# Kernel optimization log

Measured on AMD Instinct MI355X. Metric: run time of the kernel, lower is better.

## Reference

```python
import jax, jax.numpy as jnp
import numpy as np

IN, H, FC1, FC2, OUT = 3, 30, 64, 32, 1
B, T = 8192, 256


def _lstm_layer(xT, W_ih, W_hh, b_ih, b_hh):
    """xT: (T, B, Din). Returns (hidden sequence (T,B,H), final h (B,H)).
    PyTorch gate order: i, f, g, o."""
    # Precompute input contribution for all timesteps (one big GEMM).
    gx = jnp.einsum('tbd,gd->tbg', xT, W_ih) + b_ih + b_hh  # (T,B,4H)
    b = xT.shape[1]
    h0 = jnp.zeros((b, W_hh.shape[1]), xT.dtype)
    c0 = h0

    def step(carry, g):
        h, c = carry
        gates = g + h @ W_hh.T
        i, f, gg, o = jnp.split(gates, 4, axis=-1)
        i = jax.nn.sigmoid(i)
        f = jax.nn.sigmoid(f)
        gg = jnp.tanh(gg)
        o = jax.nn.sigmoid(o)
        c = f * c + i * gg
        h = o * jnp.tanh(c)
        return (h, c), h

    (h_n, _), ys = jax.lax.scan(step, (h0, c0), gx)
    return ys, h_n


def setup_inputs() -> dict:
    key = jax.random.key(0)
    ks = jax.random.split(key, 16)
    s = 0.18  # ~1/sqrt(hidden_size), matches PyTorch uniform init scale
    inp = {
        'x': jax.random.normal(ks[0], (B, T, IN), jnp.float32),
        'W_ih0': jax.random.normal(ks[1], (4 * H, IN), jnp.float32) * s,
        'W_hh0': jax.random.normal(ks[2], (4 * H, H), jnp.float32) * s,
        'b_ih0': jax.random.normal(ks[3], (4 * H,), jnp.float32) * s,
        'b_hh0': jax.random.normal(ks[4], (4 * H,), jnp.float32) * s,
        'W_ih1': jax.random.normal(ks[5], (4 * H, H), jnp.float32) * s,
        'W_hh1': jax.random.normal(ks[6], (4 * H, H), jnp.float32) * s,
        'b_ih1': jax.random.normal(ks[7], (4 * H,), jnp.float32) * s,
        'b_hh1': jax.random.normal(ks[8], (4 * H,), jnp.float32) * s,
        'W_fc1': jax.random.normal(ks[9], (FC1, H), jnp.float32) * s,
        'b_fc1': jax.random.normal(ks[10], (FC1,), jnp.float32) * s,
        'W_fc2': jax.random.normal(ks[11], (FC2, FC1), jnp.float32) * 0.125,
        'b_fc2': jax.random.normal(ks[12], (FC2,), jnp.float32) * 0.125,
        'W_fc3': jax.random.normal(ks[13], (OUT, FC2), jnp.float32) * 0.17,
        'b_fc3': jax.random.normal(ks[14], (OUT,), jnp.float32) * 0.17,
    }
    return inp


def reference(x, W_ih0, W_hh0, b_ih0, b_hh0, W_ih1, W_hh1, b_ih1, b_hh1,
              W_fc1, b_fc1, W_fc2, b_fc2, W_fc3, b_fc3):
    xT = jnp.swapaxes(x, 0, 1)  # (T,B,IN)
    ys, _ = _lstm_layer(xT, W_ih0, W_hh0, b_ih0, b_hh0)   # layer 0 sequence
    _, h_n = _lstm_layer(ys, W_ih1, W_hh1, b_ih1, b_hh1)  # layer 1 final h
    # FC head (dropout = identity in eval mode)
    z = jax.nn.relu(h_n @ W_fc1.T + b_fc1)
    z = jax.nn.relu(z @ W_fc2.T + b_fc2)
    z = jax.nn.sigmoid(z @ W_fc3.T + b_fc3)
    return z.squeeze(-1)  # (B,)
```

## Files before the change

### kernel.cpp

```cpp
#include <hip/hip_runtime.h>

#define TT   256
#define HID  30
#define LOG2E 1.4426950408889634f
#define HS   56

typedef __bf16 bf16x8_t __attribute__((ext_vector_type(8)));
typedef float  f32x4_t  __attribute__((ext_vector_type(4)));

__device__ __forceinline__ float fexp2(float x){
#if __has_builtin(__builtin_amdgcn_exp2f)
    return __builtin_amdgcn_exp2f(x);
#else
    return exp2f(x);
#endif
}
__device__ __forceinline__ float frcp(float x){
#if __has_builtin(__builtin_amdgcn_rcpf)
    return __builtin_amdgcn_rcpf(x);
#else
    return 1.f/x;
#endif
}
__device__ __forceinline__ float fsigmoid(float x){ return frcp(1.f + fexp2(-LOG2E*x)); }
__device__ __forceinline__ float ftanh_f(float x){ return 2.f*frcp(1.f + fexp2(-2.f*LOG2E*x)) - 1.f; }
__device__ __forceinline__ f32x4_t exp4(f32x4_t v){
    f32x4_t e; e[0]=fexp2(v[0]); e[1]=fexp2(v[1]); e[2]=fexp2(v[2]); e[3]=fexp2(v[3]); return e;
}
__device__ __forceinline__ f32x4_t rcp4(f32x4_t v){
    f32x4_t r; r[0]=frcp(v[0]); r[1]=frcp(v[1]); r[2]=frcp(v[2]); r[3]=frcp(v[3]); return r;
}

__global__ __launch_bounds__(512, 4)
void lstm_fused(const float* __restrict__ x,
    const float* __restrict__ Wih0, const float* __restrict__ Whh0,
    const float* __restrict__ bih0, const float* __restrict__ bhh0,
    const float* __restrict__ Wih1, const float* __restrict__ Whh1,
    const float* __restrict__ bih1, const float* __restrict__ bhh1,
    const float* __restrict__ Wfc1, const float* __restrict__ bfc1,
    const float* __restrict__ Wfc2, const float* __restrict__ bfc2,
    const float* __restrict__ Wfc3, const float* __restrict__ bfc3,
    float* __restrict__ out)
{
    __shared__ __align__(16) __bf16 h0f[2][16][HS];
    __shared__ __align__(16) __bf16 h1f[2][16][HS];
    __shared__ float h1_last[16*32];
    __shared__ float zbuf[16*64];
    __shared__ float z2buf[16*32];

    const int tid  = threadIdx.x;
    const int lane = tid & 63;
    const int wvf  = tid >> 6;
    const bool grpA = (wvf < 4);
    const int wv   = wvf & 3;
    const int n    = lane & 15;
    const int q    = lane >> 4;
    const int nl   = n & 7;
    const int u    = wv*8 + nl;
    const int hi   = n >> 3;
    const bool colok = (u < HID);
    const int bbase = blockIdx.x * 16;

    const int uq  = colok ? u : 0;
    const int wr0 = (hi ? 1 : 0)*HID + uq;
    const int wr1 = (hi ? 3 : 2)*HID + uq;

    bf16x8_t fbA{}, fbB{}, fbC{}, fbD{};
    float b0=0.f, b1=0.f, wx20=0.f, wx21=0.f;
    if (grpA) {
        #pragma unroll
        for (int j = 0; j < 8; ++j) {
            int k = q*8 + j;
            float v0=0.f, v1=0.f;
            if (colok) {
                if (k < HID) { v0 = Whh0[wr0*HID+k];      v1 = Whh0[wr1*HID+k]; }
                else         { v0 = Wih0[wr0*3+(k-HID)];  v1 = Wih0[wr1*3+(k-HID)]; }
            }
            fbA[j]=(__bf16)v0; fbB[j]=(__bf16)v1;
        }
        if (colok) {
            b0 = bih0[wr0] + bhh0[wr0];
            b1 = bih0[wr1] + bhh0[wr1];
            wx20 = Wih0[wr0*3+2];  wx21 = Wih0[wr1*3+2];
        }
    } else {
        #pragma unroll
        for (int j = 0; j < 8; ++j) {
            int k = q*8 + j;
            float v0=0.f, v1=0.f, v2=0.f, v3=0.f;
            if (colok && k < HID) {
                v0 = Wih1[wr0*HID+k];  v1 = Wih1[wr1*HID+k];
                v2 = Whh1[wr0*HID+k];  v3 = Whh1[wr1*HID+k];
            }
            fbA[j]=(__bf16)v0; fbB[j]=(__bf16)v1;
            fbC[j]=(__bf16)v2; fbD[j]=(__bf16)v3;
        }
        if (colok) {
            b0 = bih1[wr0] + bhh1[wr0];
            b1 = bih1[wr1] + bhh1[wr1];
        }
    }
    const f32x4_t bv0 = {b0,b0,b0,b0};
    const f32x4_t bv1 = {b1,b1,b1,b1};
    const float mco1 = (hi==0) ? (-2.f*LOG2E) : (-LOG2E);
    const float aco1 = (hi==0) ? 2.f : 1.f;
    const float bco1 = (hi==0) ? -1.f : 0.f;

    f32x4_t cst = {0.f,0.f,0.f,0.f};

    for (int i = tid; i < 2*16*HS; i += 512) {
        (&h0f[0][0][0])[i] = (__bf16)0.f;
        (&h1f[0][0][0])[i] = (__bf16)0.f;
    }
    __syncthreads();
    if (tid < 32) {
        int m = tid >> 1, cc = tid & 1;
        h0f[1][m][30+cc] = (__bf16)x[(size_t)(bbase+m)*(TT*3) + cc];
    }
    __syncthreads();

    const float* xB = x + (size_t)bbase*(TT*3);
    const int xo2  = (q*4)*(TT*3) + 2;
    const int xo01 = (tid>>1)*(TT*3) + (tid&1);
    f32x4_t x2 = {0.f,0.f,0.f,0.f};
    if (grpA) {
        x2[0]=xB[xo2]; x2[1]=xB[xo2+TT*3]; x2[2]=xB[xo2+2*TT*3]; x2[3]=xB[xo2+3*TT*3];
    }

#define STEP(S, RB, WB, FIRST) do {                                            \
    if (grpA) {                                                                \
        bf16x8_t A0 = *(const bf16x8_t*)(&h0f[RB][n][q*8]);                    \
        f32x4_t bx0 = bv0 + x2*wx20;                                           \
        f32x4_t bx1 = bv1 + x2*wx21;                                           \
        f32x4_t a0 = __builtin_amdgcn_mfma_f32_16x16x32_bf16(A0, fbA, bx0, 0,0,0); \
        f32x4_t a1 = __builtin_amdgcn_mfma_f32_16x16x32_bf16(A0, fbB, bx1, 0,0,0); \
        const int tpre = ((S)+2 < TT) ? (S)+2 : TT-1;                          \
        const float* xs = xB + 3*tpre;                                         \
        f32x4_t x2n;                                                           \
        x2n[0]=xs[xo2]; x2n[1]=xs[xo2+TT*3];                                   \
        x2n[2]=xs[xo2+2*TT*3]; x2n[3]=xs[xo2+3*TT*3];                          \
        float x01v = 0.f;                                                      \
        if (tid < 32) x01v = xs[xo01];                                         \
        f32x4_t g0 = rcp4(exp4(a0*(-LOG2E)) + 1.f);                            \
        f32x4_t g1 = rcp4(exp4(a1*mco1) + 1.f)*aco1 + bco1;                    \
        f32x4_t p  = g0*g1;                                                    \
        p[0]=__shfl_xor(p[0],8,64); p[1]=__shfl_xor(p[1],8,64);                \
        p[2]=__shfl_xor(p[2],8,64); p[3]=__shfl_xor(p[3],8,64);                \
        cst = g0*cst + p;                                                      \
        float cA=cst[0], oA=g1[0], cB=cst[1], oB=g1[1];                        \
        float c2=__shfl_xor(cst[2],8,64), c3=__shfl_xor(cst[3],8,64);          \
        float o2=__shfl_xor(g1[2],8,64),  o3=__shfl_xor(g1[3],8,64);           \
        if (!hi) { cA=c2; oA=o2; cB=c3; oB=o3; }                               \
        float hA = oA*ftanh_f(cA);                                             \
        float hB = oB*ftanh_f(cB);                                             \
        const int row = q*4 + (hi ? 0 : 2);                                    \
        if (colok) {                                                           \
            h0f[WB][row][u]   = (__bf16)hA;                                    \
            h0f[WB][row+1][u] = (__bf16)hB;                                    \
        }                                                                      \
        if (tid < 32) h0f[WB][tid>>1][30+(tid&1)] = (__bf16)x01v;              \
        x2 = x2n;                                                              \
    } else if (!(FIRST)) {                                                     \
        bf16x8_t A1 = *(const bf16x8_t*)(&h0f[RB][n][q*8]);                    \
        bf16x8_t A2 = *(const bf16x8_t*)(&h1f[RB][n][q*8]);                    \
        f32x4_t d0 = __builtin_amdgcn_mfma_f32_16x16x32_bf16(A2, fbC, bv0, 0,0,0); \
        d0         = __builtin_amdgcn_mfma_f32_16x16x32_bf16(A1, fbA, d0,  0,0,0); \
        f32x4_t d1 = __builtin_amdgcn_mfma_f32_16x16x32_bf16(A2, fbD, bv1, 0,0,0); \
        d1         = __builtin_amdgcn_mfma_f32_16x16x32_bf16(A1, fbB, d1,  0,0,0); \
        f32x4_t g0 = rcp4(exp4(d0*(-LOG2E)) + 1.f);                            \
        f32x4_t g1 = rcp4(exp4(d1*mco1) + 1.f)*aco1 + bco1;                    \
        f32x4_t p  = g0*g1;                                                    \
        p[0]=__shfl_xor(p[0],8,64); p[1]=__shfl_xor(p[1],8,64);                \
        p[2]=__shfl_xor(p[2],8,64); p[3]=__shfl_xor(p[3],8,64);                \
        cst = g0*cst + p;                                                      \
        float cA=cst[0], oA=g1[0], cB=cst[1], oB=g1[1];                        \
        float c2=__shfl_xor(cst[2],8,64), c3=__shfl_xor(cst[3],8,64);          \
        float o2=__shfl_xor(g1[2],8,64),  o3=__shfl_xor(g1[3],8,64);           \
        if (!hi) { cA=c2; oA=o2; cB=c3; oB=o3; }                               \
        float hA = oA*ftanh_f(cA);                                             \
        float hB = oB*ftanh_f(cB);                                             \
        const int row = q*4 + (hi ? 0 : 2);                                    \
        if (colok) {                                                           \
            h1f[WB][row][u]   = (__bf16)hA;                                    \
            h1f[WB][row+1][u] = (__bf16)hB;                                    \
            if ((S) == TT-1) {                                                 \
                h1_last[row*32+u]     = hA;                                    \
                h1_last[(row+1)*32+u] = hB;                                    \
            }                                                                  \
        }                                                                      \
    }                                                                          \
    __syncthreads();                                                           \
} while (0)

    STEP(-1, 1, 0, 1);
    #pragma unroll 1
    for (int s = 0; s < TT; s += 2) {
        STEP(s,   0, 1, 0);
        STEP(s+1, 1, 0, 0);
    }
#undef STEP

    #pragma unroll
    for (int rep = 0; rep < 2; ++rep) {
        int idx = tid + rep*512;
        int m = idx >> 6, uu = idx & 63;
        float a = bfc1[uu];
        for (int k = 0; k < HID; ++k) a += h1_last[m*32+k] * Wfc1[uu*HID+k];
        zbuf[m*64+uu] = fmaxf(a, 0.f);
    }
    __syncthreads();
    {
        int m = tid >> 5, v = tid & 31;
        float a = bfc2[v];
        for (int k = 0; k < 64; ++k) a += zbuf[m*64+k] * Wfc2[v*64+k];
        z2buf[m*32+v] = fmaxf(a, 0.f);
    }
    __syncthreads();
    if (tid < 16) {
        float a = bfc3[0];
        for (int k = 0; k < 32; ++k) a += z2buf[tid*32+k] * Wfc3[k];
        out[bbase + tid] = fsigmoid(a);
    }
}

extern "C" void kernel_launch(void* const* d_in, const int* in_sizes, int n_in,
                              void* d_out, int out_size, void* d_ws, size_t ws_size,
                              hipStream_t stream) {
    const float* x    = (const float*)d_in[0];
    const float* Wih0 = (const float*)d_in[1];
    const float* Whh0 = (const float*)d_in[2];
    const float* bih0 = (const float*)d_in[3];
    const float* bhh0 = (const float*)d_in[4];
    const float* Wih1 = (const float*)d_in[5];
    const float* Whh1 = (const float*)d_in[6];
    const float* bih1 = (const float*)d_in[7];
    const float* bhh1 = (const float*)d_in[8];
    const float* Wfc1 = (const float*)d_in[9];
    const float* bfc1 = (const float*)d_in[10];
    const float* Wfc2 = (const float*)d_in[11];
    const float* bfc2 = (const float*)d_in[12];
    const float* Wfc3 = (const float*)d_in[13];
    const float* bfc3 = (const float*)d_in[14];
    float* outp = (float*)d_out;

    hipLaunchKernelGGL(lstm_fused, dim3(512), dim3(512), 0, stream,
        x, Wih0, Whh0, bih0, bhh0, Wih1, Whh1, bih1, bhh1,
        Wfc1, bfc1, Wfc2, bfc2, Wfc3, bfc3, outp);
}
```

Baseline: 327.5 us.

## Remap LSTM gates so each lane owns all four gates, halving block size

```diff
diff --git a/kernel.cpp b/kernel.cpp
--- a/kernel.cpp
+++ b/kernel.cpp
@@ -3,7 +3,7 @@
 #define TT   256
 #define HID  30
 #define LOG2E 1.4426950408889634f
-#define HS   56
+#define HS   40
 
 typedef __bf16 bf16x8_t __attribute__((ext_vector_type(8)));
 typedef float  f32x4_t  __attribute__((ext_vector_type(4)));
@@ -23,15 +23,35 @@
 #endif
 }
 __device__ __forceinline__ float fsigmoid(float x){ return frcp(1.f + fexp2(-LOG2E*x)); }
-__device__ __forceinline__ float ftanh_f(float x){ return 2.f*frcp(1.f + fexp2(-2.f*LOG2E*x)) - 1.f; }
 __device__ __forceinline__ f32x4_t exp4(f32x4_t v){
     f32x4_t e; e[0]=fexp2(v[0]); e[1]=fexp2(v[1]); e[2]=fexp2(v[2]); e[3]=fexp2(v[3]); return e;
 }
 __device__ __forceinline__ f32x4_t rcp4(f32x4_t v){
     f32x4_t r; r[0]=frcp(v[0]); r[1]=frcp(v[1]); r[2]=frcp(v[2]); r[3]=frcp(v[3]); return r;
 }
-
-__global__ __launch_bounds__(512, 4)
+__device__ __forceinline__ f32x4_t splat4(float v){ f32x4_t r = {v,v,v,v}; return r; }
+
+__device__ __forceinline__ f32x4_t lstm_act(f32x4_t aI, f32x4_t aF, f32x4_t aG,
+                                            f32x4_t aO, f32x4_t& cst){
+    f32x4_t eI = exp4(aI);
+    f32x4_t eF = exp4(aF);
+    f32x4_t eG = exp4(aG);
+    f32x4_t eO = exp4(aO);
+    f32x4_t f  = rcp4(eF + 1.f);
+    f32x4_t tG = eG + 1.f;
+    f32x4_t p  = (eG - 1.f) * rcp4(eI*tG + tG);
+    cst = f*cst + p;
+    f32x4_t cc;
+    cc[0]=fminf(fmaxf(cst[0],-30.f),30.f);
+    cc[1]=fminf(fmaxf(cst[1],-30.f),30.f);
+    cc[2]=fminf(fmaxf(cst[2],-30.f),30.f);
+    cc[3]=fminf(fmaxf(cst[3],-30.f),30.f);
+    f32x4_t eC = exp4(cc * (2.f*LOG2E));
+    f32x4_t tC = eC + 1.f;
+    return (eC - 1.f) * rcp4(eO*tC + tC);
+}
+
+__global__ __launch_bounds__(256, 2)
 void lstm_fused(const float* __restrict__ x,
     const float* __restrict__ Wih0, const float* __restrict__ Whh0,
     const float* __restrict__ bih0, const float* __restrict__ bhh0,
@@ -50,65 +70,54 @@
 
     const int tid  = threadIdx.x;
     const int lane = tid & 63;
-    const int wvf  = tid >> 6;
-    const bool grpA = (wvf < 4);
-    const int wv   = wvf & 3;
+    const int wv   = tid >> 6;
+    const int lay  = wv >> 1;
+    const int uh   = wv & 1;
     const int n    = lane & 15;
     const int q    = lane >> 4;
-    const int nl   = n & 7;
-    const int u    = wv*8 + nl;
-    const int hi   = n >> 3;
+    const int q4   = q*4;
+    const int u    = uh*16 + n;
     const bool colok = (u < HID);
+    const int uq   = colok ? u : 0;
     const int bbase = blockIdx.x * 16;
 
-    const int uq  = colok ? u : 0;
-    const int wr0 = (hi ? 1 : 0)*HID + uq;
-    const int wr1 = (hi ? 3 : 2)*HID + uq;
-
-    bf16x8_t fbA{}, fbB{}, fbC{}, fbD{};
-    float b0=0.f, b1=0.f, wx20=0.f, wx21=0.f;
-    if (grpA) {
+    bf16x8_t fA[4], fB[4];
+    float bv[4], wx[4];
+    {
+        const float scl[4] = {-LOG2E, -LOG2E, 2.f*LOG2E, -LOG2E};
         #pragma unroll
-        for (int j = 0; j < 8; ++j) {
-            int k = q*8 + j;
-            float v0=0.f, v1=0.f;
+        for (int g = 0; g < 4; ++g) {
+            const int row = g*HID + uq;
+            const float sg = scl[g];
+            bf16x8_t va{}, vb{};
+            #pragma unroll
+            for (int j = 0; j < 8; ++j) {
+                int k = q*8 + j;
+                float wa = 0.f, wb = 0.f;
+                if (colok) {
+                    if (lay == 0) {
+                        if (k < HID)      wa = Whh0[row*HID + k];
+                        else if (k < 32)  wa = Wih0[row*3 + (k - HID)];
+                    } else {
+                        if (k < HID) { wa = Wih1[row*HID + k];  wb = Whh1[row*HID + k]; }
+                    }
+                }
+                va[j] = (__bf16)(sg*wa);
+                vb[j] = (__bf16)(sg*wb);
+            }
+            fA[g] = va;  fB[g] = vb;
+            float bb = 0.f, ww = 0.f;
             if (colok) {
-                if (k < HID) { v0 = Whh0[wr0*HID+k];      v1 = Whh0[wr1*HID+k]; }
-                else         { v0 = Wih0[wr0*3+(k-HID)];  v1 = Wih0[wr1*3+(k-HID)]; }
+                bb = lay ? (bih1[row] + bhh1[row]) : (bih0[row] + bhh0[row]);
+                if (lay == 0) ww = Wih0[row*3 + 2];
             }
-            fbA[j]=(__bf16)v0; fbB[j]=(__bf16)v1;
+            bv[g] = sg*bb;  wx[g] = sg*ww;
         }
-        if (colok) {
-            b0 = bih0[wr0] + bhh0[wr0];
-            b1 = bih0[wr1] + bhh0[wr1];
-            wx20 = Wih0[wr0*3+2];  wx21 = Wih0[wr1*3+2];
-        }
-    } else {
-        #pragma unroll
-        for (int j = 0; j < 8; ++j) {
-            int k = q*8 + j;
-            float v0=0.f, v1=0.f, v2=0.f, v3=0.f;
-            if (colok && k < HID) {
-                v0 = Wih1[wr0*HID+k];  v1 = Wih1[wr1*HID+k];
-                v2 = Whh1[wr0*HID+k];  v3 = Whh1[wr1*HID+k];
-            }
-            fbA[j]=(__bf16)v0; fbB[j]=(__bf16)v1;
-            fbC[j]=(__bf16)v2; fbD[j]=(__bf16)v3;
-        }
-        if (colok) {
-            b0 = bih1[wr0] + bhh1[wr0];
-            b1 = bih1[wr1] + bhh1[wr1];
-        }
-    }
-    const f32x4_t bv0 = {b0,b0,b0,b0};
-    const f32x4_t bv1 = {b1,b1,b1,b1};
-    const float mco1 = (hi==0) ? (-2.f*LOG2E) : (-LOG2E);
-    const float aco1 = (hi==0) ? 2.f : 1.f;
-    const float bco1 = (hi==0) ? -1.f : 0.f;
+    }
 
     f32x4_t cst = {0.f,0.f,0.f,0.f};
 
-    for (int i = tid; i < 2*16*HS; i += 512) {
+    for (int i = tid; i < 2*16*HS; i += 256) {
         (&h0f[0][0][0])[i] = (__bf16)0.f;
         (&h1f[0][0][0])[i] = (__bf16)0.f;
     }
@@ -123,17 +132,17 @@
     const int xo2  = (q*4)*(TT*3) + 2;
     const int xo01 = (tid>>1)*(TT*3) + (tid&1);
     f32x4_t x2 = {0.f,0.f,0.f,0.f};
-    if (grpA) {
+    if (lay == 0) {
         x2[0]=xB[xo2]; x2[1]=xB[xo2+TT*3]; x2[2]=xB[xo2+2*TT*3]; x2[3]=xB[xo2+3*TT*3];
     }
 
 #define STEP(S, RB, WB, FIRST) do {                                            \
-    if (grpA) {                                                                \
+    if (lay == 0) {                                                            \
         bf16x8_t A0 = *(const bf16x8_t*)(&h0f[RB][n][q*8]);                    \
-        f32x4_t bx0 = bv0 + x2*wx20;                                           \
-        f32x4_t bx1 = bv1 + x2*wx21;                                           \
-        f32x4_t a0 = __builtin_amdgcn_mfma_f32_16x16x32_bf16(A0, fbA, bx0, 0,0,0); \
-        f32x4_t a1 = __builtin_amdgcn_mfma_f32_16x16x32_bf16(A0, fbB, bx1, 0,0,0); \
+        f32x4_t aI = __builtin_amdgcn_mfma_f32_16x16x32_bf16(A0, fA[0], x2*wx[0] + bv[0], 0,0,0); \
+        f32x4_t aF = __builtin_amdgcn_mfma_f32_16x16x32_bf16(A0, fA[1], x2*wx[1] + bv[1], 0,0,0); \
+        f32x4_t aG = __builtin_amdgcn_mfma_f32_16x16x32_bf16(A0, fA[2], x2*wx[2] + bv[2], 0,0,0); \
+        f32x4_t aO = __builtin_amdgcn_mfma_f32_16x16x32_bf16(A0, fA[3], x2*wx[3] + bv[3], 0,0,0); \
         const int tpre = ((S)+2 < TT) ? (S)+2 : TT-1;                          \
         const float* xs = xB + 3*tpre;                                         \
         f32x4_t x2n;                                                           \
@@ -141,51 +150,37 @@
         x2n[2]=xs[xo2+2*TT*3]; x2n[3]=xs[xo2+3*TT*3];                          \
         float x01v = 0.f;                                                      \
         if (tid < 32) x01v = xs[xo01];                                         \
-        f32x4_t g0 = rcp4(exp4(a0*(-LOG2E)) + 1.f);                            \
-        f32x4_t g1 = rcp4(exp4(a1*mco1) + 1.f)*aco1 + bco1;                    \
-        f32x4_t p  = g0*g1;                                                    \
-        p[0]=__shfl_xor(p[0],8,64); p[1]=__shfl_xor(p[1],8,64);                \
-        p[2]=__shfl_xor(p[2],8,64); p[3]=__shfl_xor(p[3],8,64);                \
-        cst = g0*cst + p;                                                      \
-        float cA=cst[0], oA=g1[0], cB=cst[1], oB=g1[1];                        \
-        float c2=__shfl_xor(cst[2],8,64), c3=__shfl_xor(cst[3],8,64);          \
-        float o2=__shfl_xor(g1[2],8,64),  o3=__shfl_xor(g1[3],8,64);           \
-        if (!hi) { cA=c2; oA=o2; cB=c3; oB=o3; }                               \
-        float hA = oA*ftanh_f(cA);                                             \
-        float hB = oB*ftanh_f(cB);                                             \
-        const int row = q*4 + (hi ? 0 : 2);                                    \
+        f32x4_t h = lstm_act(aI, aF, aG, aO, cst);                             \
         if (colok) {                                                           \
-            h0f[WB][row][u]   = (__bf16)hA;                                    \
-            h0f[WB][row+1][u] = (__bf16)hB;                                    \
+            h0f[WB][q4  ][u] = (__bf16)h[0];                                   \
+            h0f[WB][q4+1][u] = (__bf16)h[1];                                   \
+            h0f[WB][q4+2][u] = (__bf16)h[2];                                   \
+            h0f[WB][q4+3][u] = (__bf16)h[3];                                   \
         }                                                                      \
         if (tid < 32) h0f[WB][tid>>1][30+(tid&1)] = (__bf16)x01v;              \
         x2 = x2n;                                                              \
     } else if (!(FIRST)) {                                                     \
         bf16x8_t A1 = *(const bf16x8_t*)(&h0f[RB][n][q*8]);                    \
         bf16x8_t A2 = *(const bf16x8_t*)(&h1f[RB][n][q*8]);                    \
-        f32x4_t d0 = __builtin_amdgcn_mfma_f32_16x16x32_bf16(A2, fbC, bv0, 0,0,0); \
-        d0         = __builtin_amdgcn_mfma_f32_16x16x32_bf16(A1, fbA, d0,  0,0,0); \
-        f32x4_t d1 = __builtin_amdgcn_mfma_f32_16x16x32_bf16(A2, fbD, bv1, 0,0,0); \
-        d1         = __builtin_amdgcn_mfma_f32_16x16x32_bf16(A1, fbB, d1,  0,0,0); \
-        f32x4_t g0 = rcp4(exp4(d0*(-LOG2E)) + 1.f);                            \
-        f32x4_t g1 = rcp4(exp4(d1*mco1) + 1.f)*aco1 + bco1;                    \
-        f32x4_t p  = g0*g1;                                                    \
-        p[0]=__shfl_xor(p[0],8,64); p[1]=__shfl_xor(p[1],8,64);                \
-        p[2]=__shfl_xor(p[2],8,64); p[3]=__shfl_xor(p[3],8,64);                \
-        cst = g0*cst + p;                                                      \
-        float cA=cst[0], oA=g1[0], cB=cst[1], oB=g1[1];                        \
-        float c2=__shfl_xor(cst[2],8,64), c3=__shfl_xor(cst[3],8,64);          \
-        float o2=__shfl_xor(g1[2],8,64),  o3=__shfl_xor(g1[3],8,64);           \
-        if (!hi) { cA=c2; oA=o2; cB=c3; oB=o3; }                               \
-        float hA = oA*ftanh_f(cA);                                             \
-        float hB = oB*ftanh_f(cB);                                             \
-        const int row = q*4 + (hi ? 0 : 2);                                    \
+        f32x4_t aI = __builtin_amdgcn_mfma_f32_16x16x32_bf16(A2, fB[0], splat4(bv[0]), 0,0,0); \
+        aI         = __builtin_amdgcn_mfma_f32_16x16x32_bf16(A1, fA[0], aI, 0,0,0); \
+        f32x4_t aF = __builtin_amdgcn_mfma_f32_16x16x32_bf16(A2, fB[1], splat4(bv[1]), 0,0,0); \
+        aF         = __builtin_amdgcn_mfma_f32_16x16x32_bf16(A1, fA[1], aF, 0,0,0); \
+        f32x4_t aG = __builtin_amdgcn_mfma_f32_16x16x32_bf16(A2, fB[2], splat4(bv[2]), 0,0,0); \
+        aG         = __builtin_amdgcn_mfma_f32_16x16x32_bf16(A1, fA[2], aG, 0,0,0); \
+        f32x4_t aO = __builtin_amdgcn_mfma_f32_16x16x32_bf16(A2, fB[3], splat4(bv[3]), 0,0,0); \
+        aO         = __builtin_amdgcn_mfma_f32_16x16x32_bf16(A1, fA[3], aO, 0,0,0); \
+        f32x4_t h = lstm_act(aI, aF, aG, aO, cst);                             \
         if (colok) {                                                           \
-            h1f[WB][row][u]   = (__bf16)hA;                                    \
-            h1f[WB][row+1][u] = (__bf16)hB;                                    \
+            h1f[WB][q4  ][u] = (__bf16)h[0];                                   \
+            h1f[WB][q4+1][u] = (__bf16)h[1];                                   \
+            h1f[WB][q4+2][u] = (__bf16)h[2];                                   \
+            h1f[WB][q4+3][u] = (__bf16)h[3];                                   \
             if ((S) == TT-1) {                                                 \
-                h1_last[row*32+u]     = hA;                                    \
-                h1_last[(row+1)*32+u] = hB;                                    \
+                h1_last[(q4  )*32+u] = h[0];                                   \
+                h1_last[(q4+1)*32+u] = h[1];                                   \
+                h1_last[(q4+2)*32+u] = h[2];                                   \
+                h1_last[(q4+3)*32+u] = h[3];                                   \
             }                                                                  \
         }                                                                      \
     }                                                                          \
@@ -201,16 +196,18 @@
 #undef STEP
 
     #pragma unroll
-    for (int rep = 0; rep < 2; ++rep) {
-        int idx = tid + rep*512;
+    for (int rep = 0; rep < 4; ++rep) {
+        int idx = tid + rep*256;
         int m = idx >> 6, uu = idx & 63;
         float a = bfc1[uu];
         for (int k = 0; k < HID; ++k) a += h1_last[m*32+k] * Wfc1[uu*HID+k];
         zbuf[m*64+uu] = fmaxf(a, 0.f);
     }
     __syncthreads();
-    {
-        int m = tid >> 5, v = tid & 31;
+    #pragma unroll
+    for (int rep = 0; rep < 2; ++rep) {
+        int idx = tid + rep*256;
+        int m = idx >> 5, v = idx & 31;
         float a = bfc2[v];
         for (int k = 0; k < 64; ++k) a += zbuf[m*64+k] * Wfc2[v*64+k];
         z2buf[m*32+v] = fmaxf(a, 0.f);
@@ -243,7 +240,7 @@
     const float* bfc3 = (const float*)d_in[14];
     float* outp = (float*)d_out;
 
-    hipLaunchKernelGGL(lstm_fused, dim3(512), dim3(512), 0, stream,
+    hipLaunchKernelGGL(lstm_fused, dim3(512), dim3(256), 0, stream,
         x, Wih0, Whh0, bih0, bhh0, Wih1, Whh1, bih1, bhh1,
         Wfc1, bfc1, Wfc2, bfc2, Wfc3, bfc3, outp);
 }
```

Result: faster. 284.3 us (-13.2%).
